# Kernel tuning notes

Hardware: AMD Instinct MI355X
Metric: run time of the kernel (lower is better)

Reference implementation:

```python
import jax, jax.numpy as jnp
import numpy as np

N = 50000      # num nodes
E = 800000     # num edges (avg degree 16)
IN, H, OUT = 128, 128, 16
R = 8          # num relations


def rgcn_conv(x, edge_index, edge_type, W, root, bias, num_relations):
    """PyG RGCNConv with aggr='mean': out = x@root + bias + sum_r mean_{j in N_r(i)} x_j @ W_r.
    Mean is linear, so aggregate raw x_j per relation first, then one matmul per relation."""
    src, dst = edge_index[0], edge_index[1]  # messages flow src -> dst
    x_src = x[src]                            # [E, F] gather
    out = x @ root + bias                     # root/self term
    for r in range(num_relations):            # small fixed loop over relations
        m = (edge_type == r).astype(x.dtype)  # [E]
        s = jax.ops.segment_sum(x_src * m[:, None], dst, num_segments=x.shape[0])  # [N, F]
        c = jax.ops.segment_sum(m, dst, num_segments=x.shape[0])                   # [N]
        out = out + (s / jnp.maximum(c, 1.0)[:, None]) @ W[r]
    return out


def setup_inputs() -> dict:
    key = jax.random.key(0)
    ks = jax.random.split(key, 12)
    glorot = lambda k, shape: jax.random.normal(k, shape, jnp.float32) * (2.0 / (shape[-2] + shape[-1])) ** 0.5
    return {
        "x": jax.random.normal(ks[0], (N, IN), jnp.float32),
        "edge_index": jax.random.randint(ks[1], (2, E), 0, N, jnp.int64) if jax.config.read('jax_enable_x64') else jax.random.randint(ks[1], (2, E), 0, N).astype(jnp.int32),
        "edge_type": jax.random.randint(ks[2], (E,), 0, R).astype(jnp.int32),
        "w0": glorot(ks[3], (R, IN, H)),
        "root0": glorot(ks[4], (IN, H)),
        "b0": jnp.zeros((H,), jnp.float32),
        "w1": glorot(ks[5], (R, H, H)),
        "root1": glorot(ks[6], (H, H)),
        "b1": jnp.zeros((H,), jnp.float32),
        "w2": glorot(ks[7], (R, H, OUT)),
        "root2": glorot(ks[8], (H, OUT)),
        "b2": jnp.zeros((OUT,), jnp.float32),
    }


def reference(x, edge_index, edge_type, w0, root0, b0, w1, root1, b1, w2, root2, b2):
    # layer 0: in -> hidden, relu (dropout is identity in eval mode)
    h = jax.nn.relu(rgcn_conv(x, edge_index, edge_type, w0, root0, b0, R))
    # layer 1: hidden -> hidden, relu
    h = jax.nn.relu(rgcn_conv(h, edge_index, edge_type, w1, root1, b1, R))
    # layer 2: hidden -> out (no activation)
    return rgcn_conv(h, edge_index, edge_type, w2, root2, b2, R)
```

## Files before the change

kernel.cpp:

```cpp
#include <hip/hip_runtime.h>

#define N_NODES 50000
#define N_EDGES 800000
#define NREL 8
#define NB8 (N_NODES * NREL)
#define SCAN_T 12500
#define KSTEPS 36
#define A_STRIDE 1160
#define NTILES32 ((N_NODES + 31) / 32)

typedef __attribute__((ext_vector_type(8))) short short8;
typedef __attribute__((ext_vector_type(4))) float f32x4;
typedef __attribute__((ext_vector_type(2))) float f32x2;

__device__ __forceinline__ unsigned short f2bf(float v) {
    union { float f; unsigned int u; } c; c.f = v;
    return (unsigned short)((c.u + 0x7FFFu + ((c.u >> 16) & 1u)) >> 16);
}
__device__ __forceinline__ float bfhi2f(unsigned int u) {
    union { unsigned int u; float f; } c; c.u = u & 0xFFFF0000u; return c.f;
}
__device__ __forceinline__ float bflo2f(unsigned int u) {
    union { unsigned int u; float f; } c; c.u = u << 16; return c.f;
}
__device__ __forceinline__ unsigned fbits(float v) {
    union { float f; unsigned u; } c; c.f = v; return c.u;
}
__device__ __forceinline__ float bitsf(int u) {
    union { int i; float f; } c; c.i = u; return c.f;
}

#define PREP_Z   (NB8 / 4)
#define PREP_X   (N_NODES * 32)
#define PREP_P   (8 * KSTEPS * 64)
#define PREP_P2  (1 * KSTEPS * 64)
#define PREP_TOTAL (PREP_Z + PREP_X + 2 * PREP_P + PREP_P2)

__device__ __forceinline__ void pack_one(int idx, const float* __restrict__ root,
                                         const float* __restrict__ W,
                                         unsigned short* __restrict__ Wpack, int FOUT) {
    int lane = idx & 63;
    int ks = (idx >> 6) % KSTEPS;
    int ct = idx / (KSTEPS * 64);
    int kbase = ks * 32 + (lane >> 4) * 8;
    int col = ct * 16 + (lane & 15);
    union { unsigned short us[8]; uint4 v; } u;
#pragma unroll
    for (int j = 0; j < 8; j++) {
        int k = kbase + j;
        float val = (k < 128) ? root[(size_t)k * FOUT + col]
                              : W[(size_t)(k - 128) * FOUT + col];
        u.us[j] = f2bf(val);
    }
    ((uint4*)Wpack)[idx] = u.v;
}

__global__ void prep_kernel(const float* __restrict__ X, unsigned int* __restrict__ Xb2,
                            const float* __restrict__ r0, const float* __restrict__ w0,
                            unsigned short* __restrict__ Wp0,
                            const float* __restrict__ r1, const float* __restrict__ w1,
                            unsigned short* __restrict__ Wp1,
                            const float* __restrict__ r2, const float* __restrict__ w2,
                            unsigned short* __restrict__ Wp2,
                            int* __restrict__ cnt, int* __restrict__ flags) {
    int t = blockIdx.x * blockDim.x + threadIdx.x;
    if (blockIdx.x == 0 && threadIdx.x < 8) flags[threadIdx.x] = 0;
    if (t < PREP_Z) { ((int4*)cnt)[t] = make_int4(0, 0, 0, 0); return; }
    t -= PREP_Z;
    if (t < PREP_X) {
        float4 v = ((const float4*)X)[t];
        unsigned int p0 = (unsigned int)f2bf(v.x) | ((unsigned int)f2bf(v.y) << 16);
        unsigned int p1 = (unsigned int)f2bf(v.z) | ((unsigned int)f2bf(v.w) << 16);
        ((uint2*)Xb2)[t] = make_uint2(p0, p1);
        return;
    }
    t -= PREP_X;
    if (t < PREP_P) { pack_one(t, r0, w0, Wp0, 128); return; }
    t -= PREP_P;
    if (t < PREP_P) { pack_one(t, r1, w1, Wp1, 128); return; }
    t -= PREP_P;
    if (t < PREP_P2) pack_one(t, r2, w2, Wp2, 16);
}

__global__ void rank_kernel(const int* __restrict__ ei, const int* __restrict__ et,
                            int* __restrict__ cnt, int* __restrict__ rank, int E) {
    int e = blockIdx.x * blockDim.x + threadIdx.x;
    if (e >= E) return;
    int d = ei[E + e];
    int t = et[e];
    rank[e] = atomicAdd(&cnt[d * NREL + t], 1);
}

#define SCAN_BLOCKS 49
__global__ __launch_bounds__(256) void scanABC_kernel(
    const int* __restrict__ cnt, int* __restrict__ tsum, int* __restrict__ toff,
    int* __restrict__ rs8, float* __restrict__ inv8, int* __restrict__ flags) {
    int tid = threadIdx.x;
    int gstride = SCAN_BLOCKS * 256;
    for (int g = blockIdx.x * 256 + tid; g < SCAN_T; g += gstride) {
        const int4* p = (const int4*)(cnt + (size_t)g * 32);
        int s = 0;
#pragma unroll
        for (int j = 0; j < 8; j++) {
            int4 v = p[j];
            s += v.x + v.y + v.z + v.w;
        }
        tsum[g] = s;
    }
    __threadfence();
    __syncthreads();
    if (tid == 0) atomicAdd(&flags[0], 1);
    if (blockIdx.x == 0) {
        __shared__ int part[256];
        if (tid == 0) { while (atomicAdd(&flags[0], 0) < SCAN_BLOCKS) {} __threadfence(); }
        __syncthreads();
        const int C = (SCAN_T + 255) / 256;
        int n0 = tid * C, n1 = n0 + C; if (n1 > SCAN_T) n1 = SCAN_T;
        int s = 0;
        for (int n = n0; n < n1; n++) s += tsum[n];
        part[tid] = s;
        __syncthreads();
        for (int off = 1; off < 256; off <<= 1) {
            int v = (tid >= off) ? part[tid - off] : 0;
            __syncthreads();
            part[tid] += v;
            __syncthreads();
        }
        int run = (tid > 0) ? part[tid - 1] : 0;
        for (int n = n0; n < n1; n++) { toff[n] = run; run += tsum[n]; }
        __threadfence();
        __syncthreads();
        if (tid == 0) atomicAdd(&flags[1], 1);
    }
    if (tid == 0) { while (atomicAdd(&flags[1], 0) < 1) {} __threadfence(); }
    __syncthreads();
    for (int g = blockIdx.x * 256 + tid; g < SCAN_T; g += gstride) {
        int run = toff[g];
        int base = g * 32;
#pragma unroll 4
        for (int j = 0; j < 32; j++) {
            int c = cnt[base + j];
            rs8[base + j] = run;
            inv8[base + j] = 1.0f / (float)(c > 0 ? c : 1);
            run += c;
        }
    }
    if (blockIdx.x == 0 && tid == 0) rs8[NB8] = N_EDGES;
}

__global__ void place_kernel(const int* __restrict__ ei, const int* __restrict__ et,
                             const int* __restrict__ rank, const int* __restrict__ rs8,
                             unsigned short* __restrict__ csr_src, int E) {
    int e = blockIdx.x * blockDim.x + threadIdx.x;
    if (e >= E) return;
    int s = ei[e];
    int d = ei[E + e];
    int t = et[e];
    csr_src[rs8[d * NREL + t] + rank[e]] = (unsigned short)s;
}

template <int FOUT, bool RELU>
__global__ __launch_bounds__(1024, 8) void layer_kernel(
    const unsigned int* __restrict__ Xb2,
    const int* __restrict__ rs8,
    const float* __restrict__ inv8,
    const unsigned short* __restrict__ csr_src,
    const unsigned short* __restrict__ Wpack,
    const float* __restrict__ bias,
    void* __restrict__ Yout)
{
    __shared__ __align__(16) unsigned short Abuf[32][A_STRIDE];

    int tid = threadIdx.x;
    int wave = tid >> 6, lane = tid & 63;
    int l15 = lane & 15;
    int node0 = blockIdx.x * 32;

    {
        int gn0 = node0 + wave * 2;
        unsigned int* row0 = (unsigned int*)&Abuf[wave * 2][0];
        unsigned int* row1 = (unsigned int*)&Abuf[wave * 2 + 1][0];

        int bl = lane <= 16 ? lane : 16;
        int bidx = gn0 * 8 + bl; if (bidx > NB8) bidx = NB8;
        int bv = rs8[bidx];
        int iidx = gn0 * 8 + l15; if (iidx > NB8 - 1) iidx = NB8 - 1;
        int invi = ((const int*)inv8)[iidx];
        unsigned sidx0 = (unsigned)(gn0 < N_NODES - 1 ? gn0 : N_NODES - 1);
        unsigned int self0 = Xb2[(sidx0 << 6) | lane];
        unsigned int self1 = Xb2[((sidx0 + 1) << 6) | lane];

        int e     = __builtin_amdgcn_readlane(bv, 0);
        int e_end = __builtin_amdgcn_readlane(bv, 16);

        row0[lane] = self0;
        row1[lane] = self1;

        int r = 0;
        int be = __builtin_amdgcn_readlane(bv, 1);
        f32x2 av = (f32x2){0.f, 0.f};

#define FLUSH_R()                                                              \
        do {                                                                   \
            float iv_ = bitsf(__builtin_amdgcn_readlane(invi, r));             \
            unsigned ux_ = fbits(av.x * iv_) + 0x8000u;                        \
            unsigned uy_ = fbits(av.y * iv_) + 0x8000u;                        \
            unsigned pk_ = __builtin_amdgcn_perm(uy_, ux_, 0x07060302u);       \
            unsigned int* rw_ = (r < 8) ? row0 : row1;                         \
            rw_[(1 + (r & 7)) * 64 + lane] = pk_;                              \
            av = (f32x2){0.f, 0.f}; r++;                                       \
            be = __builtin_amdgcn_readlane(bv, r + 1 <= 16 ? r + 1 : 16);      \
        } while (0)

        if (e < e_end) {
            int e1m = e_end - 1;
            int ma = e + lane; if (ma > e1m) ma = e1m;
            unsigned int mv = csr_src[ma];
            int wbase = e;
            while (e < e_end) {
                int bn = e_end - e; if (bn > 16) bn = 16;
                int koff = e - wbase;
                int sc[16];
#pragma unroll
                for (int k = 0; k < 16; k++)
                    sc[k] = __builtin_amdgcn_readlane((int)mv, koff + k);
                unsigned int xp[16];
#pragma unroll
                for (int k = 0; k < 16; k++)
                    xp[k] = Xb2[((unsigned)sc[k] << 6) | lane];
                int en = e + bn;
                if (koff + bn == 64 && en < e_end) {
                    int mb = en + lane; if (mb > e1m) mb = e1m;
                    mv = csr_src[mb];
                    wbase = en;
                }
#pragma unroll
                for (int k = 0; k < 16; k++) {
                    if (k < bn) {
                        int ec = e + k;
                        while (ec >= be) FLUSH_R();
                        av += (f32x2){bflo2f(xp[k]), bfhi2f(xp[k])};
                    }
                }
                e = en;
            }
        }
        while (r < 16) FLUSH_R();
#undef FLUSH_R
    }
    __syncthreads();

    int quad = lane >> 4, l16 = lane & 15;
    if constexpr (FOUT == 128) {
        int ct = wave & 7;
        int half = wave >> 3;
        int node0h = node0 + half * 16;
        f32x4 acc = (f32x4){0.f, 0.f, 0.f, 0.f};
        const unsigned short* arow = &Abuf[half * 16 + l16][0];
        for (int ks = 0; ks < KSTEPS; ks++) {
            short8 b = *(const short8*)(Wpack + (((size_t)ct * KSTEPS + ks) * 64 + lane) * 8);
            short8 a = *(const short8*)(arow + ks * 32 + quad * 8);
            acc = __builtin_amdgcn_mfma_f32_16x16x32_bf16(a, b, acc, 0, 0, 0);
        }
        unsigned short* Yb = (unsigned short*)Yout;
        int h = ct * 16 + l16;
        float bvs = bias[h];
#pragma unroll
        for (int r4 = 0; r4 < 4; r4++) {
            int node = node0h + quad * 4 + r4;
            if (node < N_NODES) {
                float v = acc[r4] + bvs;
                if (RELU) v = v > 0.f ? v : 0.f;
                Yb[(size_t)node * 128 + h] = f2bf(v);
            }
        }
    } else {
        int half = wave >> 3, w8 = wave & 7;
        int ks0 = w8 * 4 + (w8 < 4 ? w8 : 4);
        int ksn = (w8 < 4) ? 5 : 4;
        f32x4 acc = (f32x4){0.f, 0.f, 0.f, 0.f};
        const unsigned short* arow = &Abuf[half * 16 + l16][0];
        for (int ks = ks0; ks < ks0 + ksn; ks++) {
            short8 b = *(const short8*)(Wpack + ((size_t)ks * 64 + lane) * 8);
            short8 a = *(const short8*)(arow + ks * 32 + quad * 8);
            acc = __builtin_amdgcn_mfma_f32_16x16x32_bf16(a, b, acc, 0, 0, 0);
        }
        __syncthreads();
        float* red = (float*)&Abuf[0][0];
#pragma unroll
        for (int r4 = 0; r4 < 4; r4++)
            red[(((half * 8 + w8) * 64 + lane) << 2) + r4] = acc[r4];
        __syncthreads();
        if (tid < 512) {
            int half2 = tid >> 8, reg = (tid >> 6) & 3, l = tid & 63;
            float s = 0.f;
#pragma unroll
            for (int w = 0; w < 8; w++)
                s += red[(((half2 * 8 + w) * 64 + l) << 2) + reg];
            int node = node0 + half2 * 16 + ((l >> 4) << 2) + reg;
            int h = l & 15;
            if (node < N_NODES) {
                float v = s + bias[h];
                if (RELU) v = v > 0.f ? v : 0.f;
                ((float*)Yout)[(size_t)node * 16 + h] = v;
            }
        }
    }
}

extern "C" void kernel_launch(void* const* d_in, const int* in_sizes, int n_in,
                              void* d_out, int out_size, void* d_ws, size_t ws_size,
                              hipStream_t stream) {
    const float* x  = (const float*)d_in[0];
    const int*   ei = (const int*)d_in[1];
    const int*   et = (const int*)d_in[2];
    const float* w0 = (const float*)d_in[3];
    const float* r0 = (const float*)d_in[4];
    const float* b0 = (const float*)d_in[5];
    const float* w1 = (const float*)d_in[6];
    const float* r1 = (const float*)d_in[7];
    const float* b1 = (const float*)d_in[8];
    const float* w2 = (const float*)d_in[9];
    const float* r2 = (const float*)d_in[10];
    const float* b2 = (const float*)d_in[11];

    char* wsp = (char*)d_ws;
    size_t off = 0;
    auto alloc = [&](size_t bytes) -> void* {
        void* p = wsp + off;
        off += (bytes + 255) & ~(size_t)255;
        return p;
    };

    int* cnt    = (int*)alloc((size_t)NB8 * 4);
    int* rs8    = (int*)alloc(((size_t)NB8 + 1) * 4);
    float* inv8 = (float*)alloc((size_t)NB8 * 4);
    int* rank   = (int*)alloc((size_t)N_EDGES * 4);
    int* tsum   = (int*)alloc((size_t)SCAN_T * 4);
    int* toff   = (int*)alloc((size_t)SCAN_T * 4);
    int* flags  = (int*)alloc(8 * 4);
    unsigned short* csr_src = (unsigned short*)alloc((size_t)N_EDGES * 2);
    unsigned short* Wp0 = (unsigned short*)alloc((size_t)8 * KSTEPS * 64 * 8 * 2);
    unsigned short* Wp1 = (unsigned short*)alloc((size_t)8 * KSTEPS * 64 * 8 * 2);
    unsigned short* Wp2 = (unsigned short*)alloc((size_t)1 * KSTEPS * 64 * 8 * 2);
    unsigned int* Xb = (unsigned int*)alloc((size_t)N_NODES * 64 * 4);
    unsigned int* H0 = (unsigned int*)alloc((size_t)N_NODES * 64 * 4);
    unsigned int* H1 = (unsigned int*)alloc((size_t)N_NODES * 64 * 4);

    prep_kernel<<<dim3((PREP_TOTAL + 255) / 256), dim3(256), 0, stream>>>(
        x, Xb, r0, w0, Wp0, r1, w1, Wp1, r2, w2, Wp2, cnt, flags);
    rank_kernel<<<dim3((N_EDGES + 255) / 256), dim3(256), 0, stream>>>(ei, et, cnt, rank, N_EDGES);
    scanABC_kernel<<<dim3(SCAN_BLOCKS), dim3(256), 0, stream>>>(cnt, tsum, toff, rs8, inv8, flags);
    place_kernel<<<dim3((N_EDGES + 255) / 256), dim3(256), 0, stream>>>(ei, et, rank, rs8,
                                                                        csr_src, N_EDGES);

    layer_kernel<128, true ><<<dim3(NTILES32), dim3(1024), 0, stream>>>(
        Xb, rs8, inv8, csr_src, Wp0, b0, (void*)H0);
    layer_kernel<128, true ><<<dim3(NTILES32), dim3(1024), 0, stream>>>(
        H0, rs8, inv8, csr_src, Wp1, b1, (void*)H1);
    layer_kernel<16, false><<<dim3(NTILES32), dim3(1024), 0, stream>>>(
        H1, rs8, inv8, csr_src, Wp2, b2, d_out);
}
```

Measured before the change: 343.4 us.

## Fuse CSR build into one persistent kernel and double-buffer edge gathers

Merges the rank, scan and place kernels into a single persistent kernel of 104 blocks that uses global atomic barriers with s_sleep between phases, removing two kernel launches. The layer kernel's edge aggregation loop now ping-pongs two 16-entry register buffers, so the gathers for the next chunk are issued before the current chunk is accumulated. This hides gather latency at the cost of more registers. The software grid barrier relies on all 104 blocks being co-resident, and the fused kernel has far fewer threads for the edge-parallel phases.

```diff
diff --git a/kernel.cpp b/kernel.cpp
--- a/kernel.cpp
+++ b/kernel.cpp
@@ -8,6 +8,7 @@
 #define KSTEPS 36
 #define A_STRIDE 1160
 #define NTILES32 ((N_NODES + 31) / 32)
+#define BB 104
 
 typedef __attribute__((ext_vector_type(8))) short short8;
 typedef __attribute__((ext_vector_type(4))) float f32x4;
@@ -82,22 +83,39 @@
     if (t < PREP_P2) pack_one(t, r2, w2, Wp2, 16);
 }
 
-__global__ void rank_kernel(const int* __restrict__ ei, const int* __restrict__ et,
-                            int* __restrict__ cnt, int* __restrict__ rank, int E) {
-    int e = blockIdx.x * blockDim.x + threadIdx.x;
-    if (e >= E) return;
-    int d = ei[E + e];
-    int t = et[e];
-    rank[e] = atomicAdd(&cnt[d * NREL + t], 1);
-}
-
-#define SCAN_BLOCKS 49
-__global__ __launch_bounds__(256) void scanABC_kernel(
-    const int* __restrict__ cnt, int* __restrict__ tsum, int* __restrict__ toff,
-    int* __restrict__ rs8, float* __restrict__ inv8, int* __restrict__ flags) {
+__device__ __forceinline__ void sleep_wait(int* flag, int target) {
+    while (atomicAdd(flag, 0) < target) __builtin_amdgcn_s_sleep(2);
+    __threadfence();
+}
+__device__ __forceinline__ void gbar(int* flag, int n, int tid) {
+    __syncthreads();
+    if (tid == 0) {
+        __threadfence();
+        atomicAdd(flag, 1);
+        sleep_wait(flag, n);
+    }
+    __syncthreads();
+}
+
+__global__ __launch_bounds__(256) void build_kernel(
+    const int* __restrict__ ei, const int* __restrict__ et,
+    int* __restrict__ cnt, int* __restrict__ rank,
+    int* __restrict__ tsum, int* __restrict__ toff,
+    int* __restrict__ rs8, float* __restrict__ inv8,
+    unsigned short* __restrict__ csr_src, int* __restrict__ flags)
+{
     int tid = threadIdx.x;
-    int gstride = SCAN_BLOCKS * 256;
-    for (int g = blockIdx.x * 256 + tid; g < SCAN_T; g += gstride) {
+    int gid = blockIdx.x * 256 + tid;
+    const int T = BB * 256;
+
+    for (int e = gid; e < N_EDGES; e += T) {
+        int d = ei[N_EDGES + e];
+        int ty = et[e];
+        rank[e] = atomicAdd(&cnt[d * NREL + ty], 1);
+    }
+    gbar(&flags[0], BB, tid);
+
+    for (int g = gid; g < SCAN_T; g += T) {
         const int4* p = (const int4*)(cnt + (size_t)g * 32);
         int s = 0;
 #pragma unroll
@@ -107,13 +125,10 @@
         }
         tsum[g] = s;
     }
-    __threadfence();
-    __syncthreads();
-    if (tid == 0) atomicAdd(&flags[0], 1);
+    gbar(&flags[1], BB, tid);
+
     if (blockIdx.x == 0) {
         __shared__ int part[256];
-        if (tid == 0) { while (atomicAdd(&flags[0], 0) < SCAN_BLOCKS) {} __threadfence(); }
-        __syncthreads();
         const int C = (SCAN_T + 255) / 256;
         int n0 = tid * C, n1 = n0 + C; if (n1 > SCAN_T) n1 = SCAN_T;
         int s = 0;
@@ -130,11 +145,12 @@
         for (int n = n0; n < n1; n++) { toff[n] = run; run += tsum[n]; }
         __threadfence();
         __syncthreads();
-        if (tid == 0) atomicAdd(&flags[1], 1);
-    }
-    if (tid == 0) { while (atomicAdd(&flags[1], 0) < 1) {} __threadfence(); }
+        if (tid == 0) atomicAdd(&flags[2], 1);
+    }
+    if (tid == 0) sleep_wait(&flags[2], 1);
     __syncthreads();
-    for (int g = blockIdx.x * 256 + tid; g < SCAN_T; g += gstride) {
+
+    for (int g = gid; g < SCAN_T; g += T) {
         int run = toff[g];
         int base = g * 32;
 #pragma unroll 4
@@ -145,18 +161,15 @@
             run += c;
         }
     }
-    if (blockIdx.x == 0 && tid == 0) rs8[NB8] = N_EDGES;
-}
-
-__global__ void place_kernel(const int* __restrict__ ei, const int* __restrict__ et,
-                             const int* __restrict__ rank, const int* __restrict__ rs8,
-                             unsigned short* __restrict__ csr_src, int E) {
-    int e = blockIdx.x * blockDim.x + threadIdx.x;
-    if (e >= E) return;
-    int s = ei[e];
-    int d = ei[E + e];
-    int t = et[e];
-    csr_src[rs8[d * NREL + t] + rank[e]] = (unsigned short)s;
+    if (gid == 0) rs8[NB8] = N_EDGES;
+    gbar(&flags[3], BB, tid);
+
+    for (int e = gid; e < N_EDGES; e += T) {
+        int s = ei[e];
+        int d = ei[N_EDGES + e];
+        int ty = et[e];
+        csr_src[rs8[d * NREL + ty] + rank[e]] = (unsigned short)s;
+    }
 }
 
 template <int FOUT, bool RELU>
@@ -217,32 +230,49 @@
             int ma = e + lane; if (ma > e1m) ma = e1m;
             unsigned int mv = csr_src[ma];
             int wbase = e;
-            while (e < e_end) {
-                int bn = e_end - e; if (bn > 16) bn = 16;
-                int koff = e - wbase;
-                int sc[16];
-#pragma unroll
-                for (int k = 0; k < 16; k++)
-                    sc[k] = __builtin_amdgcn_readlane((int)mv, koff + k);
-                unsigned int xp[16];
-#pragma unroll
-                for (int k = 0; k < 16; k++)
-                    xp[k] = Xb2[((unsigned)sc[k] << 6) | lane];
-                int en = e + bn;
-                if (koff + bn == 64 && en < e_end) {
-                    int mb = en + lane; if (mb > e1m) mb = e1m;
+
+            unsigned int xpA[16], xpB[16];
+
+            auto issue = [&](unsigned int (&xp)[16], int epos) {
+                int koff = epos - wbase;
+                if (koff == 64) {
+                    int mb = epos + lane; if (mb > e1m) mb = e1m;
                     mv = csr_src[mb];
-                    wbase = en;
+                    wbase = epos;
+                    koff = 0;
                 }
+#pragma unroll
+                for (int k = 0; k < 16; k++) {
+                    int sck = __builtin_amdgcn_readlane((int)mv, koff + k);
+                    xp[k] = Xb2[((unsigned)sck << 6) | lane];
+                }
+            };
+            auto accum = [&](unsigned int (&xp)[16], int epos, int bn) {
 #pragma unroll
                 for (int k = 0; k < 16; k++) {
                     if (k < bn) {
-                        int ec = e + k;
+                        int ec = epos + k;
                         while (ec >= be) FLUSH_R();
                         av += (f32x2){bflo2f(xp[k]), bfhi2f(xp[k])};
                     }
                 }
-                e = en;
+            };
+
+            int bnA = e_end - e; if (bnA > 16) bnA = 16;
+            issue(xpA, e);
+            while (true) {
+                int eB = e + bnA;
+                int bnB = e_end - eB; if (bnB > 16) bnB = 16;
+                if (bnB > 0) issue(xpB, eB);
+                accum(xpA, e, bnA);
+                e = eB;
+                if (bnB <= 0) break;
+                int eA = e + bnB;
+                bnA = e_end - eA; if (bnA > 16) bnA = 16;
+                if (bnA > 0) issue(xpA, eA);
+                accum(xpB, e, bnB);
+                e = eA;
+                if (bnA <= 0) break;
             }
         }
         while (r < 16) FLUSH_R();
@@ -349,10 +379,8 @@
 
     prep_kernel<<<dim3((PREP_TOTAL + 255) / 256), dim3(256), 0, stream>>>(
         x, Xb, r0, w0, Wp0, r1, w1, Wp1, r2, w2, Wp2, cnt, flags);
-    rank_kernel<<<dim3((N_EDGES + 255) / 256), dim3(256), 0, stream>>>(ei, et, cnt, rank, N_EDGES);
-    scanABC_kernel<<<dim3(SCAN_BLOCKS), dim3(256), 0, stream>>>(cnt, tsum, toff, rs8, inv8, flags);
-    place_kernel<<<dim3((N_EDGES + 255) / 256), dim3(256), 0, stream>>>(ei, et, rank, rs8,
-                                                                        csr_src, N_EDGES);
+    build_kernel<<<dim3(BB), dim3(256), 0, stream>>>(
+        ei, et, cnt, rank, tsum, toff, rs8, inv8, csr_src, flags);
 
     layer_kernel<128, true ><<<dim3(NTILES32), dim3(1024), 0, stream>>>(
         Xb, rs8, inv8, csr_src, Wp0, b0, (void*)H0);
```

New measurement: 371.5 us. 1.08x slower.
